# Kernel tuning notes

Measured on AMD Instinct MI355X. Metric: run time of the kernel, lower is better.

The kernel has to match this reference:

```python
import jax, jax.numpy as jnp
import numpy as np

FILTER_SIZE = 8
INPUT_DIM = 128
KERNEL_SIZE = 256


def setup_inputs() -> dict:
    key = jax.random.key(0)
    k1, k2, k3, k4 = jax.random.split(key, 4)
    user_batch = jax.random.normal(k1, (32, 2048, INPUT_DIM), dtype=jnp.float32)
    # Params initialized like torch.rand (uniform [0,1))
    filt = jax.random.uniform(k2, (FILTER_SIZE, INPUT_DIM), dtype=jnp.float32)
    W_k = jax.random.uniform(k3, (FILTER_SIZE * INPUT_DIM, KERNEL_SIZE), dtype=jnp.float32)
    b_k = jax.random.uniform(k4, (KERNEL_SIZE,), dtype=jnp.float32)
    return {"user_batch": user_batch, "filt": filt, "W_k": W_k, "b_k": b_k}


def reference(user_batch, filt, W_k, b_k):
    B, L, D = user_batch.shape
    F = filt.shape[0]
    n_win = L - F  # NOTE: original loop is range(0, L - F): exactly L - F windows
    # Gather sliding windows: [B, n_win, F, D]
    idx = jnp.arange(n_win)[:, None] + jnp.arange(F)[None, :]
    windows = user_batch[:, idx, :]
    # Elementwise mul with filter then contract flattened (F*D) against W_k
    W = W_k.reshape(F, D, -1)  # [F, D, K]
    out = jnp.einsum('blfd,fd,fdk->blk', windows, filt, W)
    return jax.nn.relu(out + b_k)
```

## Files before the change

kernel.cpp:

```cpp
#include <hip/hip_runtime.h>


#define L_SZ   2048
#define NWIN   2040
#define BM     128
#define MT     16

typedef __attribute__((ext_vector_type(8)))  short bf16x8;
typedef __attribute__((ext_vector_type(4)))  short bf16x4;
typedef __attribute__((ext_vector_type(16))) float f32x16;

static __device__ __forceinline__ short f2bf(float f) {
    union { float f; unsigned u; } v; v.f = f;
    unsigned r = v.u + 0x7FFFu + ((v.u >> 16) & 1u);
    return (short)(r >> 16);
}

static __device__ __forceinline__ void gload_lds16(const short* g, short* l) {
    __builtin_amdgcn_global_load_lds(
        (const __attribute__((address_space(1))) unsigned int*)g,
        (__attribute__((address_space(3))) unsigned int*)l, 16, 0, 0);
}

__global__ __launch_bounds__(256) void prep_w_kernel(
    const float* __restrict__ Wk, const float* __restrict__ filt,
    short* __restrict__ wp4)
{
    int g    = blockIdx.x * 256 + threadIdx.x;
    int c16  = g >> 9;
    int s    = g & 511;
    int half = s >> 8;
    int n    = s & 255;
    int kb   = c16 * 16 + half * 8;
    bf16x8 o;
    #pragma unroll
    for (int jj = 0; jj < 8; ++jj)
        o[jj] = f2bf(Wk[(size_t)(kb + jj) * 256 + n] * filt[kb + jj]);
    *reinterpret_cast<bf16x8*>(&wp4[(size_t)g * 8]) = o;
}

__global__ __launch_bounds__(512, 4) void cnn_enc_kernel(
    const float* __restrict__ ub, const short* __restrict__ wp4,
    const float* __restrict__ bk, float* __restrict__ out)
{
    __shared__ short sA[135 * 136];
    __shared__ short sB[4 * 4096];

    const int tid   = threadIdx.x;
    const int bid   = blockIdx.x;
    const int mt    = bid & 15;
    const int batch = bid >> 4;
    const int l0    = mt * BM;

    const int lane = tid & 63;
    const int wave = tid >> 6;
    const int wm   = wave >> 2;
    const int wn   = wave & 3;
    const int l32  = lane & 31;
    const int half = lane >> 5;

    auto stageB = [&](int c) {
        const short* src = wp4 + (size_t)c * 4096 + (size_t)(wave * 64 + lane) * 8;
        gload_lds16(src, &sB[(c & 3) * 4096 + wave * 512]);
    };

    const float* ubb = ub + ((size_t)batch << 18);
    float4 av[9];
    #pragma unroll
    for (int u = 0; u < 9; ++u) {
        int idx = tid + u * 512;
        if (u < 8 || idx < 4320) {
            int r  = idx >> 5;
            int c4 = idx & 31;
            int rg = l0 + r; if (rg > L_SZ - 1) rg = L_SZ - 1;
            av[u] = *reinterpret_cast<const float4*>(
                ubb + ((size_t)rg << 7) + c4 * 4);
        }
    }
    stageB(0); stageB(1); stageB(2);
    #pragma unroll
    for (int u = 0; u < 9; ++u) {
        int idx = tid + u * 512;
        if (u < 8 || idx < 4320) {
            int r  = idx >> 5;
            int c4 = idx & 31;
            bf16x4 o;
            o.x = f2bf(av[u].x); o.y = f2bf(av[u].y);
            o.z = f2bf(av[u].z); o.w = f2bf(av[u].w);
            *reinterpret_cast<bf16x4*>(&sA[r * 136 + c4 * 4]) = o;
        }
    }

    f32x16 acc[2][2];
    #pragma unroll
    for (int i = 0; i < 2; ++i)
        #pragma unroll
        for (int j = 0; j < 2; ++j)
            acc[i][j] = (f32x16){0.f,0.f,0.f,0.f,0.f,0.f,0.f,0.f,
                                 0.f,0.f,0.f,0.f,0.f,0.f,0.f,0.f};

    int aoff[2];
    #pragma unroll
    for (int i = 0; i < 2; ++i)
        aoff[i] = (wm * 64 + i * 32 + l32) * 136 + half * 8;
    const int boff = (half * 256 + wn * 64 + l32) * 8;

    asm volatile("s_waitcnt vmcnt(2) lgkmcnt(0)" ::: "memory");
    __builtin_amdgcn_s_barrier();
    __builtin_amdgcn_sched_barrier(0);

    #pragma unroll 1
    for (int c = 0; c < 64; ++c) {
        const int f = c >> 3, dsub = c & 7;
        const int bb = (c & 3) * 4096;
        bf16x8 a0 = *reinterpret_cast<const bf16x8*>(
            &sA[aoff[0] + f * 136 + dsub * 16]);
        bf16x8 a1 = *reinterpret_cast<const bf16x8*>(
            &sA[aoff[1] + f * 136 + dsub * 16]);
        bf16x8 b0 = *reinterpret_cast<const bf16x8*>(&sB[bb + boff]);
        bf16x8 b1 = *reinterpret_cast<const bf16x8*>(&sB[bb + boff + 256]);
        if (c < 63) {
            if (c < 62) asm volatile("s_waitcnt vmcnt(1)" ::: "memory");
            else        asm volatile("s_waitcnt vmcnt(0)" ::: "memory");
            __builtin_amdgcn_s_barrier();
            __builtin_amdgcn_sched_barrier(0);
            if (c < 61) stageB(c + 3);
        }
        __builtin_amdgcn_s_setprio(1);
        acc[0][0] = __builtin_amdgcn_mfma_f32_32x32x16_bf16(a0, b0, acc[0][0], 0, 0, 0);
        acc[0][1] = __builtin_amdgcn_mfma_f32_32x32x16_bf16(a0, b1, acc[0][1], 0, 0, 0);
        acc[1][0] = __builtin_amdgcn_mfma_f32_32x32x16_bf16(a1, b0, acc[1][0], 0, 0, 0);
        acc[1][1] = __builtin_amdgcn_mfma_f32_32x32x16_bf16(a1, b1, acc[1][1], 0, 0, 0);
        __builtin_amdgcn_s_setprio(0);
    }

    #pragma unroll
    for (int j = 0; j < 2; ++j) {
        int n_glob = wn * 64 + j * 32 + l32;
        float bias = bk[n_glob];
        #pragma unroll
        for (int i = 0; i < 2; ++i) {
            #pragma unroll
            for (int r = 0; r < 16; ++r) {
                int row = (r & 3) + 8 * (r >> 2) + 4 * half;
                int l = l0 + wm * 64 + i * 32 + row;
                if (l < NWIN) {
                    float v = acc[i][j][r] + bias;
                    __builtin_nontemporal_store(
                        v > 0.f ? v : 0.f,
                        &out[((size_t)batch * NWIN + l) * 256 + n_glob]);
                }
            }
        }
    }
}

extern "C" void kernel_launch(void* const* d_in, const int* in_sizes, int n_in,
                              void* d_out, int out_size, void* d_ws, size_t ws_size,
                              hipStream_t stream) {
    const float* ub   = (const float*)d_in[0];
    const float* filt = (const float*)d_in[1];
    const float* Wk   = (const float*)d_in[2];
    const float* bk   = (const float*)d_in[3];
    float* out = (float*)d_out;
    short* wp4 = (short*)d_ws;

    hipLaunchKernelGGL(prep_w_kernel, dim3(128), dim3(256), 0, stream,
                       Wk, filt, wp4);
    hipLaunchKernelGGL(cnn_enc_kernel, dim3(32 * MT), dim3(512), 0, stream,
                       ub, wp4, bk, out);
}
```

Measured before the change: 124.7 us.

## Halve M-tile to 64 rows and use double-buffered B staging for occupancy

Shrinks the per-block row tile from 128 to 64, doubling the grid to 1024 blocks. Each wave now computes a single 32-row by 64-column slice with two accumulators instead of four. LDS use drops (smaller A window, B ring cut from four slots to two), and launch bounds now request 8 blocks per SM. The hand-tuned vmcnt waits, three-deep prefetch and setprio are replaced by a simple one-ahead prefetch with a full __syncthreads each iteration. This trades A-tile reuse, and brings more B reloads and barriers, for higher occupancy and better load spreading.

```diff
diff --git a/kernel.cpp b/kernel.cpp
--- a/kernel.cpp
+++ b/kernel.cpp
@@ -3,8 +3,8 @@
 
 #define L_SZ   2048
 #define NWIN   2040
-#define BM     128
-#define MT     16
+#define BM     64
+#define MT     32
 
 typedef __attribute__((ext_vector_type(8)))  short bf16x8;
 typedef __attribute__((ext_vector_type(4)))  short bf16x4;
@@ -39,17 +39,17 @@
     *reinterpret_cast<bf16x8*>(&wp4[(size_t)g * 8]) = o;
 }
 
-__global__ __launch_bounds__(512, 4) void cnn_enc_kernel(
+__global__ __launch_bounds__(512, 8) void cnn_enc_kernel(
     const float* __restrict__ ub, const short* __restrict__ wp4,
     const float* __restrict__ bk, float* __restrict__ out)
 {
-    __shared__ short sA[135 * 136];
-    __shared__ short sB[4 * 4096];
+    __shared__ short sA[71 * 136];
+    __shared__ short sB[2 * 4096];
 
     const int tid   = threadIdx.x;
     const int bid   = blockIdx.x;
-    const int mt    = bid & 15;
-    const int batch = bid >> 4;
+    const int mt    = bid & 31;
+    const int batch = bid >> 5;
     const int l0    = mt * BM;
 
     const int lane = tid & 63;
@@ -60,96 +60,76 @@
     const int half = lane >> 5;
 
     auto stageB = [&](int c) {
-        const short* src = wp4 + (size_t)c * 4096 + (size_t)(wave * 64 + lane) * 8;
-        gload_lds16(src, &sB[(c & 3) * 4096 + wave * 512]);
+        const short* src = wp4 + (size_t)c * 4096 + (size_t)tid * 8;
+        gload_lds16(src, &sB[(c & 1) * 4096 + wave * 512]);
     };
 
-    const float* ubb = ub + ((size_t)batch << 18);
-    float4 av[9];
-    #pragma unroll
-    for (int u = 0; u < 9; ++u) {
-        int idx = tid + u * 512;
-        if (u < 8 || idx < 4320) {
-            int r  = idx >> 5;
-            int c4 = idx & 31;
-            int rg = l0 + r; if (rg > L_SZ - 1) rg = L_SZ - 1;
-            av[u] = *reinterpret_cast<const float4*>(
-                ubb + ((size_t)rg << 7) + c4 * 4);
+    {
+        const float* ubb = ub + ((size_t)batch << 18);
+        float4 av[5];
+        #pragma unroll
+        for (int u = 0; u < 5; ++u) {
+            int idx = tid + u * 512;
+            if (u < 4 || idx < 2272) {
+                int r  = idx >> 5;
+                int c4 = idx & 31;
+                int rg = l0 + r; if (rg > L_SZ - 1) rg = L_SZ - 1;
+                av[u] = *reinterpret_cast<const float4*>(
+                    ubb + ((size_t)rg << 7) + c4 * 4);
+            }
         }
-    }
-    stageB(0); stageB(1); stageB(2);
-    #pragma unroll
-    for (int u = 0; u < 9; ++u) {
-        int idx = tid + u * 512;
-        if (u < 8 || idx < 4320) {
-            int r  = idx >> 5;
-            int c4 = idx & 31;
-            bf16x4 o;
-            o.x = f2bf(av[u].x); o.y = f2bf(av[u].y);
-            o.z = f2bf(av[u].z); o.w = f2bf(av[u].w);
-            *reinterpret_cast<bf16x4*>(&sA[r * 136 + c4 * 4]) = o;
+        stageB(0);
+        #pragma unroll
+        for (int u = 0; u < 5; ++u) {
+            int idx = tid + u * 512;
+            if (u < 4 || idx < 2272) {
+                int r  = idx >> 5;
+                int c4 = idx & 31;
+                bf16x4 o;
+                o.x = f2bf(av[u].x); o.y = f2bf(av[u].y);
+                o.z = f2bf(av[u].z); o.w = f2bf(av[u].w);
+                *reinterpret_cast<bf16x4*>(&sA[r * 136 + c4 * 4]) = o;
+            }
         }
     }
 
-    f32x16 acc[2][2];
-    #pragma unroll
-    for (int i = 0; i < 2; ++i)
-        #pragma unroll
-        for (int j = 0; j < 2; ++j)
-            acc[i][j] = (f32x16){0.f,0.f,0.f,0.f,0.f,0.f,0.f,0.f,
-                                 0.f,0.f,0.f,0.f,0.f,0.f,0.f,0.f};
+    f32x16 acc0 = (f32x16){0.f,0.f,0.f,0.f,0.f,0.f,0.f,0.f,
+                           0.f,0.f,0.f,0.f,0.f,0.f,0.f,0.f};
+    f32x16 acc1 = acc0;
 
-    int aoff[2];
-    #pragma unroll
-    for (int i = 0; i < 2; ++i)
-        aoff[i] = (wm * 64 + i * 32 + l32) * 136 + half * 8;
+    const int aoff = (wm * 32 + l32) * 136 + half * 8;
     const int boff = (half * 256 + wn * 64 + l32) * 8;
 
-    asm volatile("s_waitcnt vmcnt(2) lgkmcnt(0)" ::: "memory");
-    __builtin_amdgcn_s_barrier();
-    __builtin_amdgcn_sched_barrier(0);
+    __syncthreads();
 
     #pragma unroll 1
     for (int c = 0; c < 64; ++c) {
+        if (c < 63) stageB(c + 1);
         const int f = c >> 3, dsub = c & 7;
-        const int bb = (c & 3) * 4096;
-        bf16x8 a0 = *reinterpret_cast<const bf16x8*>(
-            &sA[aoff[0] + f * 136 + dsub * 16]);
-        bf16x8 a1 = *reinterpret_cast<const bf16x8*>(
-            &sA[aoff[1] + f * 136 + dsub * 16]);
+        const int bb = (c & 1) * 4096;
+        bf16x8 a = *reinterpret_cast<const bf16x8*>(
+            &sA[aoff + f * 136 + dsub * 16]);
         bf16x8 b0 = *reinterpret_cast<const bf16x8*>(&sB[bb + boff]);
         bf16x8 b1 = *reinterpret_cast<const bf16x8*>(&sB[bb + boff + 256]);
-        if (c < 63) {
-            if (c < 62) asm volatile("s_waitcnt vmcnt(1)" ::: "memory");
-            else        asm volatile("s_waitcnt vmcnt(0)" ::: "memory");
-            __builtin_amdgcn_s_barrier();
-            __builtin_amdgcn_sched_barrier(0);
-            if (c < 61) stageB(c + 3);
-        }
-        __builtin_amdgcn_s_setprio(1);
-        acc[0][0] = __builtin_amdgcn_mfma_f32_32x32x16_bf16(a0, b0, acc[0][0], 0, 0, 0);
-        acc[0][1] = __builtin_amdgcn_mfma_f32_32x32x16_bf16(a0, b1, acc[0][1], 0, 0, 0);
-        acc[1][0] = __builtin_amdgcn_mfma_f32_32x32x16_bf16(a1, b0, acc[1][0], 0, 0, 0);
-        acc[1][1] = __builtin_amdgcn_mfma_f32_32x32x16_bf16(a1, b1, acc[1][1], 0, 0, 0);
-        __builtin_amdgcn_s_setprio(0);
+        acc0 = __builtin_amdgcn_mfma_f32_32x32x16_bf16(a, b0, acc0, 0, 0, 0);
+        acc1 = __builtin_amdgcn_mfma_f32_32x32x16_bf16(a, b1, acc1, 0, 0, 0);
+        __syncthreads();
     }
 
     #pragma unroll
     for (int j = 0; j < 2; ++j) {
         int n_glob = wn * 64 + j * 32 + l32;
         float bias = bk[n_glob];
+        const f32x16& acc = j ? acc1 : acc0;
         #pragma unroll
-        for (int i = 0; i < 2; ++i) {
-            #pragma unroll
-            for (int r = 0; r < 16; ++r) {
-                int row = (r & 3) + 8 * (r >> 2) + 4 * half;
-                int l = l0 + wm * 64 + i * 32 + row;
-                if (l < NWIN) {
-                    float v = acc[i][j][r] + bias;
-                    __builtin_nontemporal_store(
-                        v > 0.f ? v : 0.f,
-                        &out[((size_t)batch * NWIN + l) * 256 + n_glob]);
-                }
+        for (int r = 0; r < 16; ++r) {
+            int row = (r & 3) + 8 * (r >> 2) + 4 * half;
+            int l = l0 + wm * 32 + row;
+            if (l < NWIN) {
+                float v = acc[r] + bias;
+                __builtin_nontemporal_store(
+                    v > 0.f ? v : 0.f,
+                    &out[((size_t)batch * NWIN + l) * 256 + n_glob]);
             }
         }
     }
```

New measurement: 131.0 us. +5.1%, slower.
